# Performance work log

Hardware: AMD Instinct MI355X
Metric: run time of the kernel (lower is better)

The kernel has to match this reference:

```python
import jax, jax.numpy as jnp
import numpy as np
import math

B, N, D_MODEL, H = 4, 2048, 1024, 16
D_HEAD = D_MODEL // H

def setup_inputs() -> dict:
    key = jax.random.key(0)
    ks = jax.random.split(key, 9)
    s = 1.0 / math.sqrt(D_MODEL)
    inp = {
        "X_Q": jax.random.normal(ks[0], (B, N, D_MODEL), jnp.float32),
        "X_K": jax.random.normal(ks[1], (B, N, D_MODEL), jnp.float32),
        "X_V": jax.random.normal(ks[2], (B, N, D_MODEL), jnp.float32),
        # stacked per-head projection weights: [H, D_MODEL, D_HEAD] (y = x @ W + b)
        "Wq": jax.random.uniform(ks[3], (H, D_MODEL, D_HEAD), jnp.float32, -s, s),
        "Wk": jax.random.uniform(ks[4], (H, D_MODEL, D_HEAD), jnp.float32, -s, s),
        "Wv": jax.random.uniform(ks[5], (H, D_MODEL, D_HEAD), jnp.float32, -s, s),
        "bq": jax.random.uniform(ks[6], (H, D_HEAD), jnp.float32, -s, s),
        "bk": jax.random.uniform(ks[7], (H, D_HEAD), jnp.float32, -s, s),
        "bv": jax.random.uniform(ks[8], (H, D_HEAD), jnp.float32, -s, s),
    }
    return inp

def reference(X_Q, X_K, X_V, Wq, Wk, Wv, bq, bk, bv):
    # per-head projections, batched over heads: [B, H, N, D_HEAD]
    Q = jnp.einsum("bnd,hde->bhne", X_Q, Wq) + bq[None, :, None, :]
    K = jnp.einsum("bnd,hde->bhne", X_K, Wk) + bk[None, :, None, :]
    V = jnp.einsum("bnd,hde->bhne", X_V, Wv) + bv[None, :, None, :]
    scores = jnp.einsum("bhne,bhme->bhnm", Q, K)  # [B, H, N, N]
    # causal (att_mask=True): mask strictly-upper-triangular with -inf
    causal = jnp.tril(jnp.ones((N, N), dtype=bool))
    scores = jnp.where(causal[None, None], scores, -jnp.inf)
    # original divides AFTER masking; -inf stays -inf so equivalent
    probs = jax.nn.softmax(scores / math.sqrt(D_HEAD), axis=-1)
    out = jnp.einsum("bhnm,bhme->bhne", probs, V)  # [B, H, N, D_HEAD]
    # concat heads along feature dim
    return out.transpose(0, 2, 1, 3).reshape(B, N, D_MODEL)
```

## Files before the change

kernel.cpp:

```cpp
#include <hip/hip_runtime.h>

typedef _Float16 half8  __attribute__((ext_vector_type(8)));
typedef _Float16 half4v __attribute__((ext_vector_type(4)));
typedef _Float16 half2v __attribute__((ext_vector_type(2)));
typedef float    floatx4 __attribute__((ext_vector_type(4)));

#define B_   4
#define N_   2048
#define DM_  1024
#define H_   16
#define DH_  64

static const size_t XEL = (size_t)B_ * N_ * DM_;
static const size_t WEL = (size_t)DM_ * DM_;
static const size_t QEL = (size_t)B_ * H_ * N_ * DH_;

#define GLOAD_LDS16(src, dst) \
  __builtin_amdgcn_global_load_lds((const __attribute__((address_space(1))) void*)(src), \
                                   (__attribute__((address_space(3))) void*)(dst), 16, 0, 0)

#define SBAR0() __builtin_amdgcn_sched_barrier(0)

__global__ void cvt_w(const float* __restrict__ w0, const float* __restrict__ w1,
                      const float* __restrict__ w2, _Float16* __restrict__ out) {
  const int z = blockIdx.z;
  const float* w = (z == 0) ? w0 : (z == 1 ? w1 : w2);
  _Float16* o = out + (size_t)z * WEL;
  const int idx = blockIdx.x * 256 + threadIdx.x;
  const int n = idx >> 10, k = idx & 1023;
  const int h = n >> 6, e = n & 63;
  o[idx] = (_Float16)w[((size_t)h * 1024 + k) * 64 + e];
}

__global__ __launch_bounds__(256, 4) void qkv_gemm(const float* __restrict__ XQ32,
                                                   const float* __restrict__ XK32,
                                                   const float* __restrict__ XV32,
                                                   const _Float16* __restrict__ W16t,
                                                   const float* __restrict__ b0,
                                                   const float* __restrict__ b1,
                                                   const float* __restrict__ b2,
                                                   _Float16* __restrict__ QK,
                                                   _Float16* __restrict__ Vt) {
  __shared__ char smem[40960];
  const int lid = blockIdx.x;
  const int win = lid >> 6;
  const int i6  = lid & 63;
  const int n0i = i6 >> 3;
  const int c   = i6 & 7;
  const int g   = win * 8 + c;
  const int z   = g >> 6;
  const int row0 = (g & 63) * 128;
  const int n0   = n0i * 128;

  const float* X32 = (z == 0) ? XQ32 : (z == 1 ? XK32 : XV32);
  const _Float16* W = W16t + (size_t)z * WEL;
  const float* bias = (z == 0) ? b0 : (z == 1 ? b1 : b2);
  const float osc = (z == 0) ? 0.18033688011112042f : 1.0f;
  _Float16* out = QK + (size_t)z * QEL;

  const int tid = threadIdx.x;
  const int w   = tid >> 6;
  const int l   = tid & 63;
  const int lg  = l >> 4, lr = l & 15;
  const int wm  = w >> 1, wn = w & 1;

  floatx4 zf = {0.f, 0.f, 0.f, 0.f};
  floatx4 acc[4][4];
#pragma unroll
  for (int mi = 0; mi < 4; ++mi)
#pragma unroll
    for (int ni = 0; ni < 4; ++ni) acc[mi][ni] = zf;

  floatx4 xr[2][2];
  auto XLOAD = [&](int kt) {
    const int k0 = kt * 32;
#pragma unroll
    for (int i = 0; i < 2; ++i) {
      const int C = i * 256 + tid, row = C >> 2, cj = C & 3;
      const int kc = cj ^ ((row >> 1) & 3);
      const float* p = X32 + (size_t)(row0 + row) * 1024 + k0 + kc * 8;
      xr[i][0] = *(const floatx4*)p;
      xr[i][1] = *(const floatx4*)(p + 4);
    }
  };
  auto XWRITE = [&](int bufc) {
    char* Ab = smem + bufc * 8192;
#pragma unroll
    for (int i = 0; i < 2; ++i) {
      const int C = i * 256 + tid, row = C >> 2, cj = C & 3;
      half8 hv;
#pragma unroll
      for (int u = 0; u < 4; ++u) {
        hv[u]     = (_Float16)xr[i][0][u];
        hv[4 + u] = (_Float16)xr[i][1][u];
      }
      *(half8*)(Ab + row * 64 + cj * 16) = hv;
    }
  };
  auto WSTAGE = [&](int kt, int bufc) {
    char* Bb = smem + 16384 + bufc * 8192;
    const int k0 = kt * 32;
#pragma unroll
    for (int i = 0; i < 2; ++i) {
      const int q   = i * 4 + w;
      const int row = q * 16 + (l >> 2);
      const int kb  = (l & 3) ^ ((row >> 1) & 3);
      GLOAD_LDS16(W + (size_t)(n0 + row) * 1024 + k0 + kb * 8, Bb + q * 1024);
    }
  };

  const int chq = (lg ^ ((lr >> 1) & 3)) * 16;
  const int aA  = wm * 4096 + lr * 64 + chq;
  const int aB  = 16384 + wn * 4096 + lr * 64 + chq;

  XLOAD(0);
  XWRITE(0);
  SBAR0();
  WSTAGE(0, 0);
  SBAR0();
  WSTAGE(1, 1);
  SBAR0();
  XLOAD(1);
  SBAR0();
  asm volatile("s_waitcnt vmcnt(6) lgkmcnt(0)" ::: "memory");
  SBAR0();
  __builtin_amdgcn_s_barrier();
  SBAR0();

  int rb = 0, wb = 2;
  for (int kt = 0; kt < 32; ++kt) {
    const int cur = kt & 1, nxt = cur ^ 1;

    if (kt + 1 < 32) {
      XWRITE(nxt);
      SBAR0();
      if (kt + 2 < 32) {
        WSTAGE(kt + 2, wb);
        SBAR0();
        XLOAD(kt + 2);
        SBAR0();
      }
    }

    const char* Al = smem + cur * 8192;
    const char* Bl = smem + rb * 8192;
    half8 af[4], bf[4];
#pragma unroll
    for (int mi = 0; mi < 4; ++mi) af[mi] = *(const half8*)(Al + aA + mi * 1024);
#pragma unroll
    for (int ni = 0; ni < 4; ++ni) bf[ni] = *(const half8*)(Bl + aB + ni * 1024);
#pragma unroll
    for (int mi = 0; mi < 4; ++mi)
#pragma unroll
      for (int ni = 0; ni < 4; ++ni)
        acc[mi][ni] = __builtin_amdgcn_mfma_f32_16x16x32_f16(af[mi], bf[ni], acc[mi][ni], 0, 0, 0);

    if (kt + 1 < 32) {
      SBAR0();
      if (kt + 2 < 32) {
        asm volatile("s_waitcnt vmcnt(6) lgkmcnt(0)" ::: "memory");
      } else {
        asm volatile("s_waitcnt vmcnt(0) lgkmcnt(0)" ::: "memory");
      }
      SBAR0();
      __builtin_amdgcn_s_barrier();
      SBAR0();
    }
    rb = (rb == 2) ? 0 : rb + 1;
    wb = (wb == 2) ? 0 : wb + 1;
  }

  if (z == 2) {
#pragma unroll
    for (int mi = 0; mi < 4; ++mi)
#pragma unroll
      for (int ni = 0; ni < 4; ++ni) {
        const int gc = n0 + wn * 64 + ni * 16 + lr;
        const float bv = bias[gc];
        const int h = gc >> 6, e = gc & 63;
        const int nb = row0 + wm * 64 + mi * 16 + lg * 4;
        const int bb = nb >> 11, nn = nb & 2047;
        half4v hv;
#pragma unroll
        for (int j = 0; j < 4; ++j) hv[j] = (_Float16)(acc[mi][ni][j] + bv);
        *(half4v*)(Vt + ((size_t)(bb * 16 + h) * 64 + e) * 2048 + nn) = hv;
      }
  } else {
#pragma unroll
    for (int mi = 0; mi < 4; ++mi)
#pragma unroll
      for (int ni = 0; ni < 4; ++ni) {
        const int gc = n0 + wn * 64 + ni * 16 + lr;
        const float bv = bias[gc];
        const int h = gc >> 6, e = gc & 63;
#pragma unroll
        for (int j = 0; j < 4; ++j) {
          const int gr = row0 + wm * 64 + mi * 16 + lg * 4 + j;
          const int b = gr >> 11, n = gr & 2047;
          out[(((size_t)(b * 16 + h)) * 2048 + n) * 64 + e] = (_Float16)((acc[mi][ni][j] + bv) * osc);
        }
      }
  }
}

__global__ __launch_bounds__(512, 4) void attn(const _Float16* __restrict__ Q16,
                                               const _Float16* __restrict__ K16,
                                               const _Float16* __restrict__ Vt16,
                                               float* __restrict__ out) {
  __shared__ char smem[49152];
  const int lid = blockIdx.x;
  const int bh = (lid & 7) | ((lid >> 6) << 3);
  const int bx = (lid >> 3) & 7;
  const int tid = threadIdx.x;
  const int w = tid >> 6, l = tid & 63;
  const int lg = l >> 4, lr = l & 15;
  const int b = bh >> 4, h = bh & 15;

  const int sz = lr & 7;
  const int aK0 = lr * 128 + ((lg ^ sz) * 16);
  const int aK1 = lr * 128 + (((4 + lg) ^ sz) * 16);
  const int pbase = 32768 + w * 2048 + lr * 128;
  int aPw[4];
#pragma unroll
  for (int cb = 0; cb < 4; ++cb)
    aPw[cb] = pbase + (((2 * cb + (lg >> 1)) ^ sz) << 4) + ((lg & 1) * 8);
  const int aPr0 = pbase + ((lg ^ sz) << 4);
  const int aPr1 = pbase + (((4 + lg) ^ sz) << 4);

  int cur = 0;

  auto STAGE = [&](int t, int bufc) {
    const int c0t = t * 64;
    char* Kb = smem + bufc * 16384;
    char* Vb = Kb + 8192;
    const int row = w * 8 + (l >> 3);
    const int kb = l & 7;
    const int ks = (kb ^ (row & 7)) << 3;
    GLOAD_LDS16(K16 + ((size_t)bh * 2048 + c0t + row) * 64 + ks, Kb + w * 1024);
    GLOAD_LDS16(Vt16 + ((size_t)bh * 64 + row) * 2048 + c0t + ks, Vb + w * 1024);
  };

  for (int ph = 0; ph < 2; ++ph) {
    const int qt = ph ? (15 - bx) : bx;
    const int q0 = qt * 128;
    const int wr0 = q0 + w * 16;
    const int nt = 2 * (qt + 1);

    half8 qf[2];
#pragma unroll
    for (int kk = 0; kk < 2; ++kk)
      qf[kk] = *(const half8*)(Q16 + ((size_t)bh * 2048 + wr0 + lr) * 64 + kk * 32 + lg * 8);

    floatx4 zf = {0.f, 0.f, 0.f, 0.f};
    floatx4 O[4];
#pragma unroll
    for (int dt = 0; dt < 4; ++dt) O[dt] = zf;
    float lden = 0.f;

    STAGE(0, cur);

    for (int t = 0; t < nt; ++t) {
      asm volatile("s_waitcnt vmcnt(0)" ::: "memory");
      __builtin_amdgcn_s_barrier();
      SBAR0();
      if (t + 1 < nt) STAGE(t + 1, cur ^ 1);
      SBAR0();

      const int c0 = t * 64;
      const char* Kb = smem + cur * 16384;

      if (c0 <= wr0 + 15) {
        floatx4 s[4];
#pragma unroll
        for (int cb = 0; cb < 4; ++cb) s[cb] = zf;
        __builtin_amdgcn_s_setprio(1);
#pragma unroll
        for (int cb = 0; cb < 4; ++cb) {
          half8 kf = *(const half8*)(Kb + aK0 + cb * 2048);
          s[cb] = __builtin_amdgcn_mfma_f32_16x16x32_f16(kf, qf[0], s[cb], 0, 0, 0);
        }
#pragma unroll
        for (int cb = 0; cb < 4; ++cb) {
          half8 kf = *(const half8*)(Kb + aK1 + cb * 2048);
          s[cb] = __builtin_amdgcn_mfma_f32_16x16x32_f16(kf, qf[1], s[cb], 0, 0, 0);
        }
        __builtin_amdgcn_s_setprio(0);

        if (c0 + 63 > wr0) {
          const int r = wr0 + lr;
#pragma unroll
          for (int cb = 0; cb < 4; ++cb)
#pragma unroll
            for (int j = 0; j < 4; ++j) {
              const int cc = c0 + cb * 16 + lg * 4 + j;
              s[cb][j] = (cc > r) ? -3.0e38f : s[cb][j];
            }
        }

        float tsum = 0.f;
#pragma unroll
        for (int cb = 0; cb < 4; ++cb)
#pragma unroll
          for (int j = 0; j < 4; ++j) {
            const float p = __builtin_amdgcn_exp2f(s[cb][j]);
            s[cb][j] = p;
            tsum += p;
          }
        tsum += __shfl_xor(tsum, 16, 64);
        tsum += __shfl_xor(tsum, 32, 64);
        lden += tsum;

#pragma unroll
        for (int cb = 0; cb < 4; ++cb) {
          half4v hv;
          hv[0] = (_Float16)s[cb][0]; hv[1] = (_Float16)s[cb][1];
          hv[2] = (_Float16)s[cb][2]; hv[3] = (_Float16)s[cb][3];
          *(half4v*)(smem + aPw[cb]) = hv;
        }
        asm volatile("s_waitcnt lgkmcnt(0)" ::: "memory");
        __builtin_amdgcn_sched_barrier(0);

        __builtin_amdgcn_s_setprio(1);
        {
          half8 pa = *(const half8*)(smem + aPr0);
#pragma unroll
          for (int dt = 0; dt < 4; ++dt) {
            half8 vb = *(const half8*)(Kb + 8192 + aK0 + dt * 2048);
            O[dt] = __builtin_amdgcn_mfma_f32_16x16x32_f16(pa, vb, O[dt], 0, 0, 0);
          }
          pa = *(const half8*)(smem + aPr1);
#pragma unroll
          for (int dt = 0; dt < 4; ++dt) {
            half8 vb = *(const half8*)(Kb + 8192 + aK1 + dt * 2048);
            O[dt] = __builtin_amdgcn_mfma_f32_16x16x32_f16(pa, vb, O[dt], 0, 0, 0);
          }
        }
        __builtin_amdgcn_s_setprio(0);
      }

      cur ^= 1;
    }

    float inv[4];
#pragma unroll
    for (int j = 0; j < 4; ++j) {
      const float lj = __shfl(lden, lg * 4 + j, 64);
      inv[j] = 1.0f / lj;
    }
#pragma unroll
    for (int dt = 0; dt < 4; ++dt)
#pragma unroll
      for (int j = 0; j < 4; ++j) {
        const int n = wr0 + lg * 4 + j;
        out[((size_t)(b * 2048 + n)) * 1024 + h * 64 + dt * 16 + lr] = O[dt][j] * inv[j];
      }
  }
}

extern "C" void kernel_launch(void* const* d_in, const int* in_sizes, int n_in,
                              void* d_out, int out_size, void* d_ws, size_t ws_size,
                              hipStream_t stream) {
  const float* XQ = (const float*)d_in[0];
  const float* XK = (const float*)d_in[1];
  const float* XV = (const float*)d_in[2];
  const float* Wq = (const float*)d_in[3];
  const float* Wk = (const float*)d_in[4];
  const float* Wv = (const float*)d_in[5];
  const float* bq = (const float*)d_in[6];
  const float* bk = (const float*)d_in[7];
  const float* bv = (const float*)d_in[8];

  char* ws = (char*)d_ws;
  _Float16* W16t = (_Float16*)(ws + 0);
  _Float16* QK   = (_Float16*)(ws + 6291456);
  _Float16* Vt   = (_Float16*)(ws + 39845888);

  cvt_w<<<dim3(4096, 1, 3), 256, 0, stream>>>(Wq, Wk, Wv, W16t);
  qkv_gemm<<<dim3(1536), 256, 0, stream>>>(XQ, XK, XV, W16t, bq, bk, bv, QK, Vt);
  attn<<<dim3(512), 512, 0, stream>>>(QK, QK + QEL, Vt, (float*)d_out);
}
```

Before: 142.9 us.

## Software-pipeline attention: overlap previous tile's PV MFMA with current softmax

Restructures the attention loop so the P·V matmul for tile t-1 is issued after the QK^T of tile t and before its exp/softmax. K/V staging moves to a triple buffer and the P staging area is double-buffered, so the previous tile's V and P stay valid. The goal is to overlap MFMA work with the exp and LDS-write latency of the softmax. The cost is shared memory growing from 48KB to 80KB, which may cut occupancy below the launch-bounds target of 4 blocks per CU, plus more code and an extra barrier per phase.

```diff
diff --git a/kernel.cpp b/kernel.cpp
--- a/kernel.cpp
+++ b/kernel.cpp
@@ -207,7 +207,7 @@
                                                const _Float16* __restrict__ K16,
                                                const _Float16* __restrict__ Vt16,
                                                float* __restrict__ out) {
-  __shared__ char smem[49152];
+  __shared__ char smem[81920];
   const int lid = blockIdx.x;
   const int bh = (lid & 7) | ((lid >> 6) << 3);
   const int bx = (lid >> 3) & 7;
@@ -219,7 +219,7 @@
   const int sz = lr & 7;
   const int aK0 = lr * 128 + ((lg ^ sz) * 16);
   const int aK1 = lr * 128 + (((4 + lg) ^ sz) * 16);
-  const int pbase = 32768 + w * 2048 + lr * 128;
+  const int pbase = 49152 + w * 4096 + lr * 128;
   int aPw[4];
 #pragma unroll
   for (int cb = 0; cb < 4; ++cb)
@@ -227,11 +227,9 @@
   const int aPr0 = pbase + ((lg ^ sz) << 4);
   const int aPr1 = pbase + (((4 + lg) ^ sz) << 4);
 
-  int cur = 0;
-
-  auto STAGE = [&](int t, int bufc) {
+  auto STAGE = [&](int t, int slot) {
     const int c0t = t * 64;
-    char* Kb = smem + bufc * 16384;
+    char* Kb = smem + slot * 16384;
     char* Vb = Kb + 8192;
     const int row = w * 8 + (l >> 3);
     const int kb = l & 7;
@@ -240,6 +238,8 @@
     GLOAD_LDS16(Vt16 + ((size_t)bh * 64 + row) * 2048 + c0t + ks, Vb + w * 1024);
   };
 
+  floatx4 zf = {0.f, 0.f, 0.f, 0.f};
+
   for (int ph = 0; ph < 2; ++ph) {
     const int qt = ph ? (15 - bx) : bx;
     const int q0 = qt * 128;
@@ -251,25 +251,29 @@
     for (int kk = 0; kk < 2; ++kk)
       qf[kk] = *(const half8*)(Q16 + ((size_t)bh * 2048 + wr0 + lr) * 64 + kk * 32 + lg * 8);
 
-    floatx4 zf = {0.f, 0.f, 0.f, 0.f};
     floatx4 O[4];
 #pragma unroll
     for (int dt = 0; dt < 4; ++dt) O[dt] = zf;
     float lden = 0.f;
-
-    STAGE(0, cur);
+    bool havePrev = false;
+
+    STAGE(0, 0);
 
     for (int t = 0; t < nt; ++t) {
       asm volatile("s_waitcnt vmcnt(0)" ::: "memory");
       __builtin_amdgcn_s_barrier();
       SBAR0();
-      if (t + 1 < nt) STAGE(t + 1, cur ^ 1);
+      if (t + 1 < nt) STAGE(t + 1, (t + 1) % 3);
       SBAR0();
 
       const int c0 = t * 64;
-      const char* Kb = smem + cur * 16384;
-
-      if (c0 <= wr0 + 15) {
+      const char* Kb = smem + (t % 3) * 16384;
+      const char* Vprev = smem + ((t + 2) % 3) * 16384 + 8192;
+      const int ppw = (t & 1) * 2048;
+      const int ppr = ((t ^ 1) & 1) * 2048;
+      const bool doQK = (c0 <= wr0 + 15);
+
+      if (doQK) {
         floatx4 s[4];
 #pragma unroll
         for (int cb = 0; cb < 4; ++cb) s[cb] = zf;
@@ -297,48 +301,100 @@
             }
         }
 
-        float tsum = 0.f;
-#pragma unroll
-        for (int cb = 0; cb < 4; ++cb)
-#pragma unroll
-          for (int j = 0; j < 4; ++j) {
-            const float p = __builtin_amdgcn_exp2f(s[cb][j]);
-            s[cb][j] = p;
-            tsum += p;
+        if (havePrev) {
+          half8 pa0 = *(const half8*)(smem + aPr0 + ppr);
+          half8 pa1 = *(const half8*)(smem + aPr1 + ppr);
+#pragma unroll
+          for (int dt = 0; dt < 4; ++dt) {
+            half8 vb = *(const half8*)(Vprev + aK0 + dt * 2048);
+            O[dt] = __builtin_amdgcn_mfma_f32_16x16x32_f16(pa0, vb, O[dt], 0, 0, 0);
           }
-        tsum += __shfl_xor(tsum, 16, 64);
-        tsum += __shfl_xor(tsum, 32, 64);
-        lden += tsum;
-
-#pragma unroll
-        for (int cb = 0; cb < 4; ++cb) {
-          half4v hv;
-          hv[0] = (_Float16)s[cb][0]; hv[1] = (_Float16)s[cb][1];
-          hv[2] = (_Float16)s[cb][2]; hv[3] = (_Float16)s[cb][3];
-          *(half4v*)(smem + aPw[cb]) = hv;
-        }
-        asm volatile("s_waitcnt lgkmcnt(0)" ::: "memory");
-        __builtin_amdgcn_sched_barrier(0);
-
+#pragma unroll
+          for (int dt = 0; dt < 4; ++dt) {
+            half8 vb = *(const half8*)(Vprev + aK1 + dt * 2048);
+            O[dt] = __builtin_amdgcn_mfma_f32_16x16x32_f16(pa1, vb, O[dt], 0, 0, 0);
+          }
+          float tsum = 0.f;
+#pragma unroll
+          for (int cb = 0; cb < 4; ++cb)
+#pragma unroll
+            for (int j = 0; j < 4; ++j) {
+              const float p = __builtin_amdgcn_exp2f(s[cb][j]);
+              s[cb][j] = p;
+              tsum += p;
+            }
+          tsum += __shfl_xor(tsum, 16, 64);
+          tsum += __shfl_xor(tsum, 32, 64);
+          lden += tsum;
+#pragma unroll
+          for (int cb = 0; cb < 4; ++cb) {
+            half4v hv;
+            hv[0] = (_Float16)s[cb][0]; hv[1] = (_Float16)s[cb][1];
+            hv[2] = (_Float16)s[cb][2]; hv[3] = (_Float16)s[cb][3];
+            *(half4v*)(smem + aPw[cb] + ppw) = hv;
+          }
+          asm volatile("s_waitcnt lgkmcnt(0)" ::: "memory");
+          SBAR0();
+        } else {
+          float tsum = 0.f;
+#pragma unroll
+          for (int cb = 0; cb < 4; ++cb)
+#pragma unroll
+            for (int j = 0; j < 4; ++j) {
+              const float p = __builtin_amdgcn_exp2f(s[cb][j]);
+              s[cb][j] = p;
+              tsum += p;
+            }
+          tsum += __shfl_xor(tsum, 16, 64);
+          tsum += __shfl_xor(tsum, 32, 64);
+          lden += tsum;
+#pragma unroll
+          for (int cb = 0; cb < 4; ++cb) {
+            half4v hv;
+            hv[0] = (_Float16)s[cb][0]; hv[1] = (_Float16)s[cb][1];
+            hv[2] = (_Float16)s[cb][2]; hv[3] = (_Float16)s[cb][3];
+            *(half4v*)(smem + aPw[cb] + ppw) = hv;
+          }
+          asm volatile("s_waitcnt lgkmcnt(0)" ::: "memory");
+          SBAR0();
+        }
+      } else if (havePrev) {
         __builtin_amdgcn_s_setprio(1);
-        {
-          half8 pa = *(const half8*)(smem + aPr0);
-#pragma unroll
-          for (int dt = 0; dt < 4; ++dt) {
-            half8 vb = *(const half8*)(Kb + 8192 + aK0 + dt * 2048);
-            O[dt] = __builtin_amdgcn_mfma_f32_16x16x32_f16(pa, vb, O[dt], 0, 0, 0);
-          }
-          pa = *(const half8*)(smem + aPr1);
-#pragma unroll
-          for (int dt = 0; dt < 4; ++dt) {
-            half8 vb = *(const half8*)(Kb + 8192 + aK1 + dt * 2048);
-            O[dt] = __builtin_amdgcn_mfma_f32_16x16x32_f16(pa, vb, O[dt], 0, 0, 0);
-          }
+        half8 pa = *(const half8*)(smem + aPr0 + ppr);
+#pragma unroll
+        for (int dt = 0; dt < 4; ++dt) {
+          half8 vb = *(const half8*)(Vprev + aK0 + dt * 2048);
+          O[dt] = __builtin_amdgcn_mfma_f32_16x16x32_f16(pa, vb, O[dt], 0, 0, 0);
+        }
+        pa = *(const half8*)(smem + aPr1 + ppr);
+#pragma unroll
+        for (int dt = 0; dt < 4; ++dt) {
+          half8 vb = *(const half8*)(Vprev + aK1 + dt * 2048);
+          O[dt] = __builtin_amdgcn_mfma_f32_16x16x32_f16(pa, vb, O[dt], 0, 0, 0);
         }
         __builtin_amdgcn_s_setprio(0);
       }
 
-      cur ^= 1;
+      havePrev = doQK;
+    }
+
+    if (havePrev) {
+      const char* Vlast = smem + ((nt - 1) % 3) * 16384 + 8192;
+      const int ppr = ((nt - 1) & 1) * 2048;
+      __builtin_amdgcn_s_setprio(1);
+      half8 pa = *(const half8*)(smem + aPr0 + ppr);
+#pragma unroll
+      for (int dt = 0; dt < 4; ++dt) {
+        half8 vb = *(const half8*)(Vlast + aK0 + dt * 2048);
+        O[dt] = __builtin_amdgcn_mfma_f32_16x16x32_f16(pa, vb, O[dt], 0, 0, 0);
+      }
+      pa = *(const half8*)(smem + aPr1 + ppr);
+#pragma unroll
+      for (int dt = 0; dt < 4; ++dt) {
+        half8 vb = *(const half8*)(Vlast + aK1 + dt * 2048);
+        O[dt] = __builtin_amdgcn_mfma_f32_16x16x32_f16(pa, vb, O[dt], 0, 0, 0);
+      }
+      __builtin_amdgcn_s_setprio(0);
     }
 
     float inv[4];
@@ -354,6 +410,9 @@
         const int n = wr0 + lg * 4 + j;
         out[((size_t)(b * 2048 + n)) * 1024 + h * 64 + dt * 16 + lr] = O[dt][j] * inv[j];
       }
+
+    __builtin_amdgcn_s_barrier();
+    SBAR0();
   }
 }
 
```

Result: slower. 147.1 us (+3.0%).
